# Optimization experiments

Hardware: AMD Instinct MI355X
Metric: run time of the kernel (lower is better)

## Reference

```python
import jax, jax.numpy as jnp
import numpy as np

D_MODEL = 1024
NUM_HEADS = 16
THETA = 10000.0
B, S = 4, 2048


def setup_inputs() -> dict:
    key = jax.random.key(0)
    ks = jax.random.split(key, 5)
    scale = 1.0 / np.sqrt(D_MODEL)  # keep logits in a sane range
    return {
        "q_proj_weight": jax.random.normal(ks[0], (D_MODEL, D_MODEL), jnp.float32) * scale,
        "k_proj_weight": jax.random.normal(ks[1], (D_MODEL, D_MODEL), jnp.float32) * scale,
        "v_proj_weight": jax.random.normal(ks[2], (D_MODEL, D_MODEL), jnp.float32) * scale,
        "o_proj_weight": jax.random.normal(ks[3], (D_MODEL, D_MODEL), jnp.float32) * scale,
        "in_features": jax.random.normal(ks[4], (B, S, D_MODEL), jnp.float32),
        "token_positions": jnp.arange(S, dtype=jnp.int32),
    }


def _rope(x, cos, sin):
    # interleaved-pair RoPE: pairs are (x[..., 2i], x[..., 2i+1])
    xe = x[..., 0::2]
    xo = x[..., 1::2]
    re = xe * cos - xo * sin
    ro = xe * sin + xo * cos
    return jnp.stack([re, ro], axis=-1).reshape(x.shape)


def reference(q_proj_weight, k_proj_weight, v_proj_weight, o_proj_weight,
              in_features, token_positions):
    Bv, Sv, _ = in_features.shape
    dk = D_MODEL // NUM_HEADS
    half = dk // 2

    q = in_features @ q_proj_weight.T
    k = in_features @ k_proj_weight.T
    v = in_features @ v_proj_weight.T
    # (B, S, D) -> (B, H, S, dk)
    q = q.reshape(Bv, Sv, NUM_HEADS, dk).transpose(0, 2, 1, 3)
    k = k.reshape(Bv, Sv, NUM_HEADS, dk).transpose(0, 2, 1, 3)
    v = v.reshape(Bv, Sv, NUM_HEADS, dk).transpose(0, 2, 1, 3)

    inv_freq = 1.0 / (THETA ** (jnp.arange(half, dtype=jnp.float32) / half))
    freqs = token_positions.astype(jnp.float32)[:, None] * inv_freq[None, :]  # (S, half)
    cos, sin = jnp.cos(freqs), jnp.sin(freqs)  # broadcast over (B, H, S, half)
    q = _rope(q, cos, sin)
    k = _rope(k, cos, sin)

    scores = jnp.einsum('bhqd,bhkd->bhqk', q, k) / np.sqrt(dk).astype(np.float32)
    causal = jnp.tril(jnp.ones((Sv, Sv), dtype=bool))
    scores = jnp.where(causal, scores, -jnp.inf)
    weights = jax.nn.softmax(scores, axis=-1)
    out = jnp.einsum('bhqk,bhkd->bhqd', weights, v)
    out = out.transpose(0, 2, 1, 3).reshape(Bv, Sv, D_MODEL)
    return out @ o_proj_weight.T
```

## Files before the change

kernel.cpp:

```cpp
#include <hip/hip_runtime.h>
#include <stdint.h>
#include <math.h>

#define NH 16
#define DK 64
#define S_LEN 2048
#define BB 4
#define DM 1024
#define M_TOT (BB*S_LEN)
#define KVT 64
#define KPAD 72
#define QB 128

#define BM 256
#define BN 128
#define BK 64
#define NTK (DM/BK)
#define LDS_A_BUF (BM*BK)
#define LDS_B_BUF (BN*BK)

typedef __attribute__((ext_vector_type(8))) short short8;
typedef __attribute__((ext_vector_type(4))) float floatx4;

typedef const __attribute__((address_space(1))) void gas_t;
typedef __attribute__((address_space(3))) void las_t;

__device__ __forceinline__ void glds16(const void* g, void* l){
  __builtin_amdgcn_global_load_lds((gas_t*)g, (las_t*)l, 16, 0, 0);
}

#define VMCNT3() asm volatile("s_waitcnt vmcnt(3)" ::: "memory")
#define VMCNT6() asm volatile("s_waitcnt vmcnt(6)" ::: "memory")
#define VMCNT0() asm volatile("s_waitcnt vmcnt(0)" ::: "memory")
#define LGKM0()  do{ asm volatile("s_waitcnt lgkmcnt(0)" ::: "memory"); __builtin_amdgcn_sched_barrier(0); }while(0)
#define BARRIER() asm volatile("s_barrier" ::: "memory")
#define SCHEDB() __builtin_amdgcn_sched_barrier(0)

__device__ __forceinline__ unsigned short f2bf(float f){
  unsigned int u = __float_as_uint(f);
  u += 0x7fffu + ((u >> 16) & 1u);
  return (unsigned short)(u >> 16);
}
__device__ __forceinline__ unsigned int pk_bf_trunc(float a, float b){
  return __builtin_amdgcn_perm(__float_as_uint(b), __float_as_uint(a), 0x07060302u);
}
__device__ __forceinline__ float fast_exp2(float x){
  return __builtin_amdgcn_exp2f(x);
}

__global__ void cast_all(const float* __restrict__ X,
                         const float* __restrict__ Wq, const float* __restrict__ Wk,
                         const float* __restrict__ Wv, const float* __restrict__ Wo,
                         unsigned short* __restrict__ Xb,
                         unsigned short* __restrict__ Wqb, unsigned short* __restrict__ Wkb,
                         unsigned short* __restrict__ Wvb, unsigned short* __restrict__ Wob)
{
  int b = blockIdx.x;
  const float* s;
  unsigned short* o;
  int base;
  if (b < 8192){ s = X; o = Xb; base = b; }
  else {
    int w = (b - 8192) >> 10;
    base = (b - 8192) & 1023;
    s = (w == 0) ? Wq : (w == 1) ? Wk : (w == 2) ? Wv : Wo;
    o = (w == 0) ? Wqb : (w == 1) ? Wkb : (w == 2) ? Wvb : Wob;
  }
  int i = base * 1024 + threadIdx.x * 4;
  float4 v = *(const float4*)(s + i);
  ushort4 u;
  u.x = f2bf(v.x); u.y = f2bf(v.y); u.z = f2bf(v.z); u.w = f2bf(v.w);
  *(ushort4*)(o + i) = u;
}

__device__ __forceinline__ void stage_part(const unsigned short* __restrict__ A,
                                           const unsigned short* __restrict__ Bm,
                                           int m0, int n0, int k0,
                                           unsigned short* As, unsigned short* Bs,
                                           int tid, int part)
{
  if (part == 0){
    #pragma unroll
    for (int j = 0; j < 2; j++){
      int c = j*512 + tid;
      int r = c >> 3;
      int sl = (c & 7) ^ (r & 7);
      glds16(&A[(size_t)(m0 + r)*DM + k0 + sl*8], (char*)As + (size_t)c*16);
    }
    int c = tid;
    int r = c >> 3;
    int sl = (c & 7) ^ (r & 7);
    glds16(&Bm[(size_t)(n0 + r)*DM + k0 + sl*8], (char*)Bs + (size_t)c*16);
  } else {
    #pragma unroll
    for (int j = 2; j < 4; j++){
      int c = j*512 + tid;
      int r = c >> 3;
      int sl = (c & 7) ^ (r & 7);
      glds16(&A[(size_t)(m0 + r)*DM + k0 + sl*8], (char*)As + (size_t)c*16);
    }
    int c = 512 + tid;
    int r = c >> 3;
    int sl = (c & 7) ^ (r & 7);
    glds16(&Bm[(size_t)(n0 + r)*DM + k0 + sl*8], (char*)Bs + (size_t)c*16);
  }
}

__device__ __forceinline__ void gemm_core(const unsigned short* __restrict__ A,
                                          const unsigned short* __restrict__ Bm,
                                          int m0, int n0, unsigned short* Ls,
                                          int tid, floatx4 (&acc)[4][4])
{
  unsigned short* AsB = Ls;
  unsigned short* BsB = Ls + 3*LDS_A_BUF;
  int wave = tid >> 6, lane = tid & 63;
  int l15 = lane & 15, quad = lane >> 4;
  int wm = (wave >> 1) * 64, wn = (wave & 1) * 64;
  int s0 = quad ^ (l15 & 7);

  short8 a01[2][2], a23[2][2], b[2][4][2];

  stage_part(A, Bm, m0, n0, 0,  AsB,             BsB,             tid, 0);
  stage_part(A, Bm, m0, n0, 0,  AsB,             BsB,             tid, 1);
  stage_part(A, Bm, m0, n0, BK, AsB + LDS_A_BUF, BsB + LDS_B_BUF, tid, 0);
  stage_part(A, Bm, m0, n0, BK, AsB + LDS_A_BUF, BsB + LDS_B_BUF, tid, 1);
  VMCNT6();
  BARRIER();
  #pragma unroll
  for (int mi = 0; mi < 2; mi++){
    const unsigned short* pr = AsB + (wm + mi*16 + l15)*BK;
    a01[mi][0] = *(const short8*)(pr + s0*8);
    a01[mi][1] = *(const short8*)(pr + (s0^4)*8);
  }
  #pragma unroll
  for (int ni = 0; ni < 4; ni++){
    const unsigned short* pr = BsB + (wn + ni*16 + l15)*BK;
    b[0][ni][0] = *(const short8*)(pr + s0*8);
    b[0][ni][1] = *(const short8*)(pr + (s0^4)*8);
  }

  #pragma unroll
  for (int t = 0; t < NTK; ++t){
    const int par = t & 1, nxt = par ^ 1;
    const unsigned short* Ab  = AsB + (t % 3)*LDS_A_BUF;
    const unsigned short* Abn = AsB + ((t+1) % 3)*LDS_A_BUF;
    const unsigned short* Bbn = BsB + ((t+1) % 3)*LDS_B_BUF;
    unsigned short* Ast = AsB + ((t+2) % 3)*LDS_A_BUF;
    unsigned short* Bst = BsB + ((t+2) % 3)*LDS_B_BUF;
    const int kst = (t + 2) * BK;

    LGKM0();
    #pragma unroll
    for (int mi = 0; mi < 2; mi++){
      const unsigned short* pr = Ab + (wm + (2+mi)*16 + l15)*BK;
      a23[mi][0] = *(const short8*)(pr + s0*8);
      a23[mi][1] = *(const short8*)(pr + (s0^4)*8);
    }
    if (t + 2 < NTK) stage_part(A, Bm, m0, n0, kst, Ast, Bst, tid, 0);
    SCHEDB();
    __builtin_amdgcn_s_setprio(1);
    #pragma unroll
    for (int kk = 0; kk < 2; kk++)
      #pragma unroll
      for (int mi = 0; mi < 2; mi++)
        #pragma unroll
        for (int ni = 0; ni < 4; ni++)
          acc[mi][ni] = __builtin_amdgcn_mfma_f32_16x16x32_bf16(a01[mi][kk], b[par][ni][kk], acc[mi][ni], 0, 0, 0);
    __builtin_amdgcn_s_setprio(0);
    if (t + 2 < NTK)      { VMCNT3(); }
    else if (t + 1 < NTK) { VMCNT0(); }
    BARRIER();

    LGKM0();
    if (t + 1 < NTK){
      #pragma unroll
      for (int mi = 0; mi < 2; mi++){
        const unsigned short* pr = Abn + (wm + mi*16 + l15)*BK;
        a01[mi][0] = *(const short8*)(pr + s0*8);
        a01[mi][1] = *(const short8*)(pr + (s0^4)*8);
      }
      #pragma unroll
      for (int ni = 0; ni < 4; ni++){
        const unsigned short* pr = Bbn + (wn + ni*16 + l15)*BK;
        b[nxt][ni][0] = *(const short8*)(pr + s0*8);
        b[nxt][ni][1] = *(const short8*)(pr + (s0^4)*8);
      }
    }
    if (t + 2 < NTK) stage_part(A, Bm, m0, n0, kst, Ast, Bst, tid, 1);
    SCHEDB();
    __builtin_amdgcn_s_setprio(1);
    #pragma unroll
    for (int kk = 0; kk < 2; kk++)
      #pragma unroll
      for (int mi = 0; mi < 2; mi++)
        #pragma unroll
        for (int ni = 0; ni < 4; ni++)
          acc[2+mi][ni] = __builtin_amdgcn_mfma_f32_16x16x32_bf16(a23[mi][kk], b[par][ni][kk], acc[2+mi][ni], 0, 0, 0);
    __builtin_amdgcn_s_setprio(0);
    if (t + 1 < NTK) BARRIER();
  }
}

__global__ __launch_bounds__(512, 2) void gemm_qkv(
    const unsigned short* __restrict__ Xb,
    const unsigned short* __restrict__ Wq,
    const unsigned short* __restrict__ Wk,
    const unsigned short* __restrict__ Wv,
    const int* __restrict__ pos,
    unsigned short* __restrict__ Qo,
    unsigned short* __restrict__ Ko,
    unsigned short* __restrict__ VTo)
{
  __shared__ __align__(16) unsigned short Ls[3*LDS_A_BUF + 3*LDS_B_BUF];
  int m0 = blockIdx.x * BM;
  int n0 = blockIdx.y * BN;
  int z  = blockIdx.z;
  const unsigned short* Bmat = (z == 0) ? Wq : ((z == 1) ? Wk : Wv);
  unsigned short* Out = (z == 0) ? Qo : ((z == 1) ? Ko : VTo);

  int tid = threadIdx.x;
  floatx4 acc[4][4] = {};
  gemm_core(Xb, Bmat, m0, n0, Ls, tid, acc);

  int wave = tid >> 6, lane = tid & 63;
  int l15 = lane & 15, quad = lane >> 4;
  int wm = (wave >> 1) * 64, wn = (wave & 1) * 64;

  if (z == 2){
    #pragma unroll
    for (int mi = 0; mi < 4; mi++){
      int row0 = m0 + wm + mi * 16 + quad * 4;
      int bb2 = row0 >> 11, sQ = row0 & (S_LEN - 1);
      #pragma unroll
      for (int ni = 0; ni < 4; ni++){
        int col = n0 + wn + ni * 16 + l15;
        int h = col >> 6, d = col & 63;
        ushort4 u;
        u.x = f2bf(acc[mi][ni][0]); u.y = f2bf(acc[mi][ni][1]);
        u.z = f2bf(acc[mi][ni][2]); u.w = f2bf(acc[mi][ni][3]);
        *(ushort4*)&Out[(((size_t)bb2 * NH + h) * DK + d) * S_LEN + sQ] = u;
      }
    }
  } else {
    const float SC = (z == 0) ? 0.180336879f : 1.0f;
    #pragma unroll
    for (int mi = 0; mi < 4; mi++){
      #pragma unroll
      for (int ni = 0; ni < 4; ni++){
        int col = n0 + wn + ni * 16 + l15;
        int h = col >> 6, d = col & 63;
        int fi = d >> 1, odd = d & 1;
        float invfrev = fast_exp2(-(float)fi * (13.2877123795494f / 32.0f)) * 0.15915494309f;
        #pragma unroll
        for (int r = 0; r < 4; r++){
          int row = m0 + wm + mi * 16 + quad * 4 + r;
          int bb2 = row >> 11, s = row & (S_LEN - 1);
          float p = (float)pos[s];
          float rev = p * invfrev;
          rev = rev - floorf(rev);
          float c  = __builtin_amdgcn_cosf(rev);
          float sn = __builtin_amdgcn_sinf(rev);
          float val = acc[mi][ni][r];
          float other = __shfl_xor(val, 1);
          float outv = odd ? (other * sn + val * c) : (val * c - other * sn);
          Out[(((size_t)bb2 * NH + h) * S_LEN + s) * DK + d] = f2bf(outv * SC);
        }
      }
    }
  }
}

__global__ __launch_bounds__(512, 2) void gemm_out(
    const unsigned short* __restrict__ Ab,
    const unsigned short* __restrict__ Wo,
    float* __restrict__ Out)
{
  __shared__ __align__(16) unsigned short Ls[3*LDS_A_BUF + 3*LDS_B_BUF];
  int m0 = blockIdx.x * BM;
  int n0 = blockIdx.y * BN;

  int tid = threadIdx.x;
  floatx4 acc[4][4] = {};
  gemm_core(Ab, Wo, m0, n0, Ls, tid, acc);

  int wave = tid >> 6, lane = tid & 63;
  int l15 = lane & 15, quad = lane >> 4;
  int wm = (wave >> 1) * 64, wn = (wave & 1) * 64;

  #pragma unroll
  for (int mi = 0; mi < 4; mi++){
    #pragma unroll
    for (int ni = 0; ni < 4; ni++){
      #pragma unroll
      for (int r = 0; r < 4; r++){
        int row = m0 + wm + mi * 16 + quad * 4 + r;
        int col = n0 + wn + ni * 16 + l15;
        Out[(size_t)row * DM + col] = acc[mi][ni][r];
      }
    }
  }
}

__global__ __launch_bounds__(256) void attn_kernel(
    const unsigned short* __restrict__ Qg,
    const unsigned short* __restrict__ Kg,
    const unsigned short* __restrict__ VTg,
    unsigned short* __restrict__ Ao)
{
  __shared__ __align__(16) unsigned short Ks[KVT * KPAD];
  __shared__ __align__(16) unsigned short Vs[DK * KPAD];
  __shared__ __align__(16) unsigned short Ps[4][32 * KPAD];

  int bh = blockIdx.x;
  int q0 = ((int)gridDim.y - 1 - (int)blockIdx.y) * QB;
  int tid = threadIdx.x, wave = tid >> 6, lane = tid & 63;
  int l15 = lane & 15, quad = lane >> 4;
  int qw = q0 + wave * 32;

  const unsigned short* Qb = Qg + (size_t)bh * S_LEN * DK;
  const unsigned short* Kb = Kg + (size_t)bh * S_LEN * DK;
  const unsigned short* Vb = VTg + (size_t)bh * DK * S_LEN;

  short8 aq[2][2];
  #pragma unroll
  for (int mi = 0; mi < 2; mi++){
    aq[mi][0] = *(const short8*)&Qb[(qw + mi * 16 + l15) * DK + quad * 8];
    aq[mi][1] = *(const short8*)&Qb[(qw + mi * 16 + l15) * DK + 32 + quad * 8];
  }

  floatx4 o[2][4] = {};
  float lsum[2][4] = {{0.f,0.f,0.f,0.f},{0.f,0.f,0.f,0.f}};

  int srow = tid >> 2;
  int scol = (tid & 3) * 16;
  int kpos = (srow & 3) * 16 + (srow >> 2);
  const unsigned short* Krow = Kb + (size_t)srow * DK + scol;
  const unsigned short* Vrow = Vb + (size_t)srow * S_LEN + scol;
  unsigned short* KsW = &Ks[kpos * KPAD + scol];
  unsigned short* VsW = &Vs[srow * KPAD + scol];

  int nt = q0 / KVT + 2;

  short8 kr0 = *(const short8*)(Krow);
  short8 kr1 = *(const short8*)(Krow + 8);
  short8 vr0 = *(const short8*)(Vrow);
  short8 vr1 = *(const short8*)(Vrow + 8);

  for (int kt = 0; kt < nt; kt++){
    int kv0 = kt * KVT;
    __syncthreads();
    *(short8*)(KsW)     = kr0;
    *(short8*)(KsW + 8) = kr1;
    *(short8*)(VsW)     = vr0;
    *(short8*)(VsW + 8) = vr1;
    if (kt + 1 < nt){
      int kvn = kv0 + KVT;
      kr0 = *(const short8*)(Krow + (size_t)kvn * DK);
      kr1 = *(const short8*)(Krow + (size_t)kvn * DK + 8);
      vr0 = *(const short8*)(Vrow + kvn);
      vr1 = *(const short8*)(Vrow + kvn + 8);
    }
    __syncthreads();

    if (kv0 <= qw + 31){
      floatx4 sc[2][4] = {};
      #pragma unroll
      for (int ni = 0; ni < 4; ni++){
        short8 bk0 = *(const short8*)&Ks[(ni * 16 + l15) * KPAD + quad * 8];
        short8 bk1 = *(const short8*)&Ks[(ni * 16 + l15) * KPAD + 32 + quad * 8];
        #pragma unroll
        for (int mi = 0; mi < 2; mi++){
          sc[mi][ni] = __builtin_amdgcn_mfma_f32_16x16x32_bf16(aq[mi][0], bk0, sc[mi][ni], 0, 0, 0);
          sc[mi][ni] = __builtin_amdgcn_mfma_f32_16x16x32_bf16(aq[mi][1], bk1, sc[mi][ni], 0, 0, 0);
        }
      }
      bool full = (kv0 + 63 <= qw);
      int kvb = kv0 + 4 * l15;
      #pragma unroll
      for (int mi = 0; mi < 2; mi++){
        #pragma unroll
        for (int r = 0; r < 4; r++){
          int qg = qw + mi * 16 + quad * 4 + r;
          float v0 = sc[mi][0][r], v1 = sc[mi][1][r], v2 = sc[mi][2][r], v3 = sc[mi][3][r];
          if (!full){
            v0 = (kvb     > qg) ? -INFINITY : v0;
            v1 = (kvb + 1 > qg) ? -INFINITY : v1;
            v2 = (kvb + 2 > qg) ? -INFINITY : v2;
            v3 = (kvb + 3 > qg) ? -INFINITY : v3;
          }
          float p0 = fast_exp2(v0);
          float p1 = fast_exp2(v1);
          float p2 = fast_exp2(v2);
          float p3 = fast_exp2(v3);
          lsum[mi][r] += (p0 + p1) + (p2 + p3);
          uint2 u;
          u.x = pk_bf_trunc(p0, p1);
          u.y = pk_bf_trunc(p2, p3);
          *(uint2*)&Ps[wave][(mi * 16 + quad * 4 + r) * KPAD + 4 * l15] = u;
        }
      }
      asm volatile("s_waitcnt lgkmcnt(0)" ::: "memory");
      short8 ap[2][2];
      #pragma unroll
      for (int mi = 0; mi < 2; mi++){
        ap[mi][0] = *(const short8*)&Ps[wave][(mi * 16 + l15) * KPAD + quad * 8];
        ap[mi][1] = *(const short8*)&Ps[wave][(mi * 16 + l15) * KPAD + 32 + quad * 8];
      }
      #pragma unroll
      for (int dt = 0; dt < 4; dt++){
        short8 bv0 = *(const short8*)&Vs[(dt * 16 + l15) * KPAD + quad * 8];
        short8 bv1 = *(const short8*)&Vs[(dt * 16 + l15) * KPAD + 32 + quad * 8];
        #pragma unroll
        for (int mi = 0; mi < 2; mi++){
          o[mi][dt] = __builtin_amdgcn_mfma_f32_16x16x32_bf16(ap[mi][0], bv0, o[mi][dt], 0, 0, 0);
          o[mi][dt] = __builtin_amdgcn_mfma_f32_16x16x32_bf16(ap[mi][1], bv1, o[mi][dt], 0, 0, 0);
        }
      }
    }
  }

  float linv[2][4];
  #pragma unroll
  for (int mi = 0; mi < 2; mi++){
    #pragma unroll
    for (int r = 0; r < 4; r++){
      float rs = lsum[mi][r];
      rs += __shfl_xor(rs, 1);
      rs += __shfl_xor(rs, 2);
      rs += __shfl_xor(rs, 4);
      rs += __shfl_xor(rs, 8);
      linv[mi][r] = 1.0f / rs;
    }
  }

  int bq = bh >> 4, hq = bh & 15;
  #pragma unroll
  for (int mi = 0; mi < 2; mi++){
    #pragma unroll
    for (int dt = 0; dt < 4; dt++){
      #pragma unroll
      for (int r = 0; r < 4; r++){
        float val = o[mi][dt][r] * linv[mi][r];
        int s = qw + mi * 16 + quad * 4 + r;
        int d = dt * 16 + l15;
        Ao[(((size_t)bq * S_LEN + s) * NH + hq) * DK + d] = f2bf(val);
      }
    }
  }
}

extern "C" void kernel_launch(void* const* d_in, const int* in_sizes, int n_in,
                              void* d_out, int out_size, void* d_ws, size_t ws_size,
                              hipStream_t stream) {
  (void)in_sizes; (void)n_in; (void)out_size; (void)ws_size;
  const float* Wq = (const float*)d_in[0];
  const float* Wk = (const float*)d_in[1];
  const float* Wv = (const float*)d_in[2];
  const float* Wo = (const float*)d_in[3];
  const float* X  = (const float*)d_in[4];
  const int* pos  = (const int*)d_in[5];
  float* out = (float*)d_out;

  char* ws = (char*)d_ws;
  const size_t MB = 1024 * 1024;
  unsigned short* Xb  = (unsigned short*)(ws);
  unsigned short* Wqb = (unsigned short*)(ws + 16 * MB);
  unsigned short* Wkb = (unsigned short*)(ws + 18 * MB);
  unsigned short* Wvb = (unsigned short*)(ws + 20 * MB);
  unsigned short* Wob = (unsigned short*)(ws + 22 * MB);
  unsigned short* Qb  = (unsigned short*)(ws + 24 * MB);
  unsigned short* Kb  = (unsigned short*)(ws + 40 * MB);
  unsigned short* Vb  = (unsigned short*)(ws + 56 * MB);
  unsigned short* Ab  = (unsigned short*)(ws + 72 * MB);

  cast_all<<<12288, 256, 0, stream>>>(X, Wq, Wk, Wv, Wo, Xb, Wqb, Wkb, Wvb, Wob);

  gemm_qkv<<<dim3(M_TOT/BM, DM/BN, 3), 512, 0, stream>>>(Xb, Wqb, Wkb, Wvb, pos, Qb, Kb, Vb);
  attn_kernel<<<dim3(64, S_LEN / QB), 256, 0, stream>>>(Qb, Kb, Vb, Ab);
  gemm_out<<<dim3(M_TOT/BM, DM/BN), 512, 0, stream>>>(Ab, Wob, out);
}
```

Baseline: 243.6 us.

## Rewrite attention with 32x32 MFMA, register-resident P, and double-buffered swizzled LDS

The attention kernel moves from 16x16x32 MFMA to 32x32x16 MFMA and computes S transposed (K times Q), so each lane owns one query row. The probability tile now stays in registers: v_permlane32_swap rearranges it into the B-operand layout, which removes the per-wave Ps LDS round trip. K and V tiles are double-buffered in XOR-swizzled unpadded LDS with a single barrier per tile, the output is written with vectorized stores, and occupancy is hinted at 3 blocks. The QKV GEMM also reorders its MFMA loops so the two k-halves of each accumulator are issued back to back, which adds a dependency chain per accumulator.

```diff
diff --git a/kernel.cpp b/kernel.cpp
--- a/kernel.cpp
+++ b/kernel.cpp
@@ -9,7 +9,6 @@
 #define DM 1024
 #define M_TOT (BB*S_LEN)
 #define KVT 64
-#define KPAD 72
 #define QB 128
 
 #define BM 256
@@ -21,6 +20,7 @@
 
 typedef __attribute__((ext_vector_type(8))) short short8;
 typedef __attribute__((ext_vector_type(4))) float floatx4;
+typedef __attribute__((ext_vector_type(16))) float floatx16;
 
 typedef const __attribute__((address_space(1))) void gas_t;
 typedef __attribute__((address_space(3))) void las_t;
@@ -35,6 +35,8 @@
 #define LGKM0()  do{ asm volatile("s_waitcnt lgkmcnt(0)" ::: "memory"); __builtin_amdgcn_sched_barrier(0); }while(0)
 #define BARRIER() asm volatile("s_barrier" ::: "memory")
 #define SCHEDB() __builtin_amdgcn_sched_barrier(0)
+
+#define PLSWAP(a, b) asm volatile("v_permlane32_swap_b32 %0, %1" : "+v"(a), "+v"(b))
 
 __device__ __forceinline__ unsigned short f2bf(float f){
   unsigned int u = __float_as_uint(f);
@@ -160,12 +162,12 @@
     SCHEDB();
     __builtin_amdgcn_s_setprio(1);
     #pragma unroll
-    for (int kk = 0; kk < 2; kk++)
-      #pragma unroll
-      for (int mi = 0; mi < 2; mi++)
-        #pragma unroll
-        for (int ni = 0; ni < 4; ni++)
-          acc[mi][ni] = __builtin_amdgcn_mfma_f32_16x16x32_bf16(a01[mi][kk], b[par][ni][kk], acc[mi][ni], 0, 0, 0);
+    for (int mi = 0; mi < 2; mi++)
+      #pragma unroll
+      for (int ni = 0; ni < 4; ni++){
+        acc[mi][ni] = __builtin_amdgcn_mfma_f32_16x16x32_bf16(a01[mi][0], b[par][ni][0], acc[mi][ni], 0, 0, 0);
+        acc[mi][ni] = __builtin_amdgcn_mfma_f32_16x16x32_bf16(a01[mi][1], b[par][ni][1], acc[mi][ni], 0, 0, 0);
+      }
     __builtin_amdgcn_s_setprio(0);
     if (t + 2 < NTK)      { VMCNT3(); }
     else if (t + 1 < NTK) { VMCNT0(); }
@@ -190,12 +192,12 @@
     SCHEDB();
     __builtin_amdgcn_s_setprio(1);
     #pragma unroll
-    for (int kk = 0; kk < 2; kk++)
-      #pragma unroll
-      for (int mi = 0; mi < 2; mi++)
-        #pragma unroll
-        for (int ni = 0; ni < 4; ni++)
-          acc[2+mi][ni] = __builtin_amdgcn_mfma_f32_16x16x32_bf16(a23[mi][kk], b[par][ni][kk], acc[2+mi][ni], 0, 0, 0);
+    for (int mi = 0; mi < 2; mi++)
+      #pragma unroll
+      for (int ni = 0; ni < 4; ni++){
+        acc[2+mi][ni] = __builtin_amdgcn_mfma_f32_16x16x32_bf16(a23[mi][0], b[par][ni][0], acc[2+mi][ni], 0, 0, 0);
+        acc[2+mi][ni] = __builtin_amdgcn_mfma_f32_16x16x32_bf16(a23[mi][1], b[par][ni][1], acc[2+mi][ni], 0, 0, 0);
+      }
     __builtin_amdgcn_s_setprio(0);
     if (t + 1 < NTK) BARRIER();
   }
@@ -301,43 +303,46 @@
   }
 }
 
-__global__ __launch_bounds__(256) void attn_kernel(
+__global__ __launch_bounds__(256, 3) void attn_kernel(
     const unsigned short* __restrict__ Qg,
     const unsigned short* __restrict__ Kg,
     const unsigned short* __restrict__ VTg,
     unsigned short* __restrict__ Ao)
 {
-  __shared__ __align__(16) unsigned short Ks[KVT * KPAD];
-  __shared__ __align__(16) unsigned short Vs[DK * KPAD];
-  __shared__ __align__(16) unsigned short Ps[4][32 * KPAD];
+  __shared__ __align__(16) unsigned short Ks[2][KVT * 64];
+  __shared__ __align__(16) unsigned short Vs[2][DK * 64];
 
   int bh = blockIdx.x;
   int q0 = ((int)gridDim.y - 1 - (int)blockIdx.y) * QB;
   int tid = threadIdx.x, wave = tid >> 6, lane = tid & 63;
-  int l15 = lane & 15, quad = lane >> 4;
+  int l31 = lane & 31, hi = lane >> 5;
   int qw = q0 + wave * 32;
+  int qg = qw + l31;
 
   const unsigned short* Qb = Qg + (size_t)bh * S_LEN * DK;
   const unsigned short* Kb = Kg + (size_t)bh * S_LEN * DK;
   const unsigned short* Vb = VTg + (size_t)bh * DK * S_LEN;
 
-  short8 aq[2][2];
-  #pragma unroll
-  for (int mi = 0; mi < 2; mi++){
-    aq[mi][0] = *(const short8*)&Qb[(qw + mi * 16 + l15) * DK + quad * 8];
-    aq[mi][1] = *(const short8*)&Qb[(qw + mi * 16 + l15) * DK + 32 + quad * 8];
-  }
-
-  floatx4 o[2][4] = {};
-  float lsum[2][4] = {{0.f,0.f,0.f,0.f},{0.f,0.f,0.f,0.f}};
-
-  int srow = tid >> 2;
-  int scol = (tid & 3) * 16;
-  int kpos = (srow & 3) * 16 + (srow >> 2);
-  const unsigned short* Krow = Kb + (size_t)srow * DK + scol;
-  const unsigned short* Vrow = Vb + (size_t)srow * S_LEN + scol;
-  unsigned short* KsW = &Ks[kpos * KPAD + scol];
-  unsigned short* VsW = &Vs[srow * KPAD + scol];
+  short8 qf[4];
+  #pragma unroll
+  for (int kc = 0; kc < 4; kc++)
+    qf[kc] = *(const short8*)&Qb[(size_t)qg * DK + kc * 16 + hi * 8];
+
+  floatx16 oA = {0.f,0.f,0.f,0.f,0.f,0.f,0.f,0.f,0.f,0.f,0.f,0.f,0.f,0.f,0.f,0.f};
+  floatx16 oB = {0.f,0.f,0.f,0.f,0.f,0.f,0.f,0.f,0.f,0.f,0.f,0.f,0.f,0.f,0.f,0.f};
+  float lsum = 0.f;
+
+  int e7 = l31 & 7;
+  int eoff[4];
+  #pragma unroll
+  for (int kc = 0; kc < 4; kc++)
+    eoff[kc] = l31 * 64 + (((kc * 2 + hi) ^ e7) * 8);
+
+  int srow = tid >> 2, sj = tid & 3;
+  const unsigned short* Krow = Kb + (size_t)srow * DK + sj * 16;
+  const unsigned short* Vrow = Vb + (size_t)srow * S_LEN + sj * 16;
+  int ws0 = (((2 * sj)     ^ (srow & 7)) * 8) + srow * 64;
+  int ws1 = (((2 * sj + 1) ^ (srow & 7)) * 8) + srow * 64;
 
   int nt = q0 / KVT + 2;
 
@@ -348,11 +353,11 @@
 
   for (int kt = 0; kt < nt; kt++){
     int kv0 = kt * KVT;
-    __syncthreads();
-    *(short8*)(KsW)     = kr0;
-    *(short8*)(KsW + 8) = kr1;
-    *(short8*)(VsW)     = vr0;
-    *(short8*)(VsW + 8) = vr1;
+    int p = kt & 1;
+    *(short8*)&Ks[p][ws0] = kr0;
+    *(short8*)&Ks[p][ws1] = kr1;
+    *(short8*)&Vs[p][ws0] = vr0;
+    *(short8*)&Vs[p][ws1] = vr1;
     if (kt + 1 < nt){
       int kvn = kv0 + KVT;
       kr0 = *(const short8*)(Krow + (size_t)kvn * DK);
@@ -360,92 +365,68 @@
       vr0 = *(const short8*)(Vrow + kvn);
       vr1 = *(const short8*)(Vrow + kvn + 8);
     }
-    __syncthreads();
-
-    if (kv0 <= qw + 31){
-      floatx4 sc[2][4] = {};
-      #pragma unroll
-      for (int ni = 0; ni < 4; ni++){
-        short8 bk0 = *(const short8*)&Ks[(ni * 16 + l15) * KPAD + quad * 8];
-        short8 bk1 = *(const short8*)&Ks[(ni * 16 + l15) * KPAD + 32 + quad * 8];
+    LGKM0();
+    BARRIER();
+
+    #pragma unroll
+    for (int sub = 0; sub < 2; sub++){
+      int kvs = kv0 + sub * 32;
+      if (kvs <= qw + 31){
+        bool subfull = (kvs + 31 <= qw);
+        floatx16 s16 = {0.f,0.f,0.f,0.f,0.f,0.f,0.f,0.f,0.f,0.f,0.f,0.f,0.f,0.f,0.f,0.f};
         #pragma unroll
-        for (int mi = 0; mi < 2; mi++){
-          sc[mi][ni] = __builtin_amdgcn_mfma_f32_16x16x32_bf16(aq[mi][0], bk0, sc[mi][ni], 0, 0, 0);
-          sc[mi][ni] = __builtin_amdgcn_mfma_f32_16x16x32_bf16(aq[mi][1], bk1, sc[mi][ni], 0, 0, 0);
+        for (int kc = 0; kc < 4; kc++){
+          short8 kf = *(const short8*)&Ks[p][sub * 2048 + eoff[kc]];
+          s16 = __builtin_amdgcn_mfma_f32_32x32x16_bf16(kf, qf[kc], s16, 0, 0, 0);
         }
-      }
-      bool full = (kv0 + 63 <= qw);
-      int kvb = kv0 + 4 * l15;
-      #pragma unroll
-      for (int mi = 0; mi < 2; mi++){
+        unsigned int u[8];
+        float ls = 0.f;
         #pragma unroll
-        for (int r = 0; r < 4; r++){
-          int qg = qw + mi * 16 + quad * 4 + r;
-          float v0 = sc[mi][0][r], v1 = sc[mi][1][r], v2 = sc[mi][2][r], v3 = sc[mi][3][r];
-          if (!full){
-            v0 = (kvb     > qg) ? -INFINITY : v0;
-            v1 = (kvb + 1 > qg) ? -INFINITY : v1;
-            v2 = (kvb + 2 > qg) ? -INFINITY : v2;
-            v3 = (kvb + 3 > qg) ? -INFINITY : v3;
+        for (int j = 0; j < 8; j++){
+          int row0 = ((2*j) & 3) + 8 * ((2*j) >> 2) + 4 * hi;
+          float v0 = s16[2*j], v1 = s16[2*j+1];
+          if (!subfull){
+            v0 = (kvs + row0     > qg) ? -INFINITY : v0;
+            v1 = (kvs + row0 + 1 > qg) ? -INFINITY : v1;
           }
           float p0 = fast_exp2(v0);
           float p1 = fast_exp2(v1);
-          float p2 = fast_exp2(v2);
-          float p3 = fast_exp2(v3);
-          lsum[mi][r] += (p0 + p1) + (p2 + p3);
-          uint2 u;
-          u.x = pk_bf_trunc(p0, p1);
-          u.y = pk_bf_trunc(p2, p3);
-          *(uint2*)&Ps[wave][(mi * 16 + quad * 4 + r) * KPAD + 4 * l15] = u;
+          ls += p0 + p1;
+          u[j] = pk_bf_trunc(p0, p1);
         }
-      }
-      asm volatile("s_waitcnt lgkmcnt(0)" ::: "memory");
-      short8 ap[2][2];
-      #pragma unroll
-      for (int mi = 0; mi < 2; mi++){
-        ap[mi][0] = *(const short8*)&Ps[wave][(mi * 16 + l15) * KPAD + quad * 8];
-        ap[mi][1] = *(const short8*)&Ps[wave][(mi * 16 + l15) * KPAD + 32 + quad * 8];
-      }
-      #pragma unroll
-      for (int dt = 0; dt < 4; dt++){
-        short8 bv0 = *(const short8*)&Vs[(dt * 16 + l15) * KPAD + quad * 8];
-        short8 bv1 = *(const short8*)&Vs[(dt * 16 + l15) * KPAD + 32 + quad * 8];
-        #pragma unroll
-        for (int mi = 0; mi < 2; mi++){
-          o[mi][dt] = __builtin_amdgcn_mfma_f32_16x16x32_bf16(ap[mi][0], bv0, o[mi][dt], 0, 0, 0);
-          o[mi][dt] = __builtin_amdgcn_mfma_f32_16x16x32_bf16(ap[mi][1], bv1, o[mi][dt], 0, 0, 0);
-        }
-      }
-    }
-  }
-
-  float linv[2][4];
-  #pragma unroll
-  for (int mi = 0; mi < 2; mi++){
-    #pragma unroll
-    for (int r = 0; r < 4; r++){
-      float rs = lsum[mi][r];
-      rs += __shfl_xor(rs, 1);
-      rs += __shfl_xor(rs, 2);
-      rs += __shfl_xor(rs, 4);
-      rs += __shfl_xor(rs, 8);
-      linv[mi][r] = 1.0f / rs;
-    }
-  }
+        lsum += ls;
+        PLSWAP(u[0], u[2]); PLSWAP(u[1], u[3]);
+        PLSWAP(u[4], u[6]); PLSWAP(u[5], u[7]);
+        union { unsigned int w[4]; short8 v; } c0, c1;
+        c0.w[0] = u[0]; c0.w[1] = u[1]; c0.w[2] = u[2]; c0.w[3] = u[3];
+        c1.w[0] = u[4]; c1.w[1] = u[5]; c1.w[2] = u[6]; c1.w[3] = u[7];
+        short8 vf0 = *(const short8*)&Vs[p][eoff[sub*2]];
+        short8 vf1 = *(const short8*)&Vs[p][eoff[sub*2+1]];
+        short8 vf2 = *(const short8*)&Vs[p][2048 + eoff[sub*2]];
+        short8 vf3 = *(const short8*)&Vs[p][2048 + eoff[sub*2+1]];
+        oA = __builtin_amdgcn_mfma_f32_32x32x16_bf16(vf0, c0.v, oA, 0, 0, 0);
+        oA = __builtin_amdgcn_mfma_f32_32x32x16_bf16(vf1, c1.v, oA, 0, 0, 0);
+        oB = __builtin_amdgcn_mfma_f32_32x32x16_bf16(vf2, c0.v, oB, 0, 0, 0);
+        oB = __builtin_amdgcn_mfma_f32_32x32x16_bf16(vf3, c1.v, oB, 0, 0, 0);
+      }
+    }
+  }
+
+  float rs = lsum + __shfl_xor(lsum, 32);
+  float linv = 1.0f / rs;
 
   int bq = bh >> 4, hq = bh & 15;
-  #pragma unroll
-  for (int mi = 0; mi < 2; mi++){
-    #pragma unroll
-    for (int dt = 0; dt < 4; dt++){
-      #pragma unroll
-      for (int r = 0; r < 4; r++){
-        float val = o[mi][dt][r] * linv[mi][r];
-        int s = qw + mi * 16 + quad * 4 + r;
-        int d = dt * 16 + l15;
-        Ao[(((size_t)bq * S_LEN + s) * NH + hq) * DK + d] = f2bf(val);
-      }
-    }
+  size_t obase = (((size_t)bq * S_LEN + qg) * NH + hq) * DK;
+  #pragma unroll
+  for (int g = 0; g < 4; g++){
+    int d0 = 8 * g + 4 * hi;
+    ushort4 ua, ub;
+    ua.x = f2bf(oA[4*g+0] * linv); ua.y = f2bf(oA[4*g+1] * linv);
+    ua.z = f2bf(oA[4*g+2] * linv); ua.w = f2bf(oA[4*g+3] * linv);
+    ub.x = f2bf(oB[4*g+0] * linv); ub.y = f2bf(oB[4*g+1] * linv);
+    ub.z = f2bf(oB[4*g+2] * linv); ub.w = f2bf(oB[4*g+3] * linv);
+    *(ushort4*)&Ao[obase + d0]      = ua;
+    *(ushort4*)&Ao[obase + 32 + d0] = ub;
   }
 }
 
```

Result: faster. 219.9 us (-9.7%).
